# Performance work log

Hardware: AMD Instinct MI355X
Metric: run time of the kernel (lower is better)

Reference implementation:

```python
import jax, jax.numpy as jnp
import numpy as np
import math

B, S, DIM = 32, 1, 4096
NH, NKV, HD = 32, 8, 128
MAXLEN = 4096
START_POS = 4095


def _rope(t, freqs):
    # t: (b, s, h, hd); freqs: (s, hd//2, 2) = (cos/real, sin/imag)
    b, s, h, hd = t.shape
    tr = t.astype(jnp.float32).reshape(b, s, h, hd // 2, 2)
    c = freqs[None, :, None, :, 0]
    sn = freqs[None, :, None, :, 1]
    x0, x1 = tr[..., 0], tr[..., 1]
    out = jnp.stack([x0 * c - x1 * sn, x0 * sn + x1 * c], axis=-1)
    return out.reshape(b, s, h, hd).astype(t.dtype)


def setup_inputs() -> dict:
    key = jax.random.key(0)
    ks = jax.random.split(key, 8)
    sd = 1.0 / math.sqrt(DIM)
    x = jax.random.normal(ks[0], (B, S, DIM), dtype=jnp.float32)
    freqs = jax.random.normal(ks[1], (S, HD // 2, 2), dtype=jnp.float32)
    cache_k = jax.random.normal(ks[2], (B, MAXLEN, NKV, HD), dtype=jnp.float32)
    cache_v = jax.random.normal(ks[3], (B, MAXLEN, NKV, HD), dtype=jnp.float32)
    wq = jax.random.normal(ks[4], (NH * HD, DIM), dtype=jnp.float32) * sd
    wk = jax.random.normal(ks[5], (NKV * HD, DIM), dtype=jnp.float32) * sd
    wv = jax.random.normal(ks[6], (NKV * HD, DIM), dtype=jnp.float32) * sd
    wo = jax.random.normal(ks[7], (DIM, NH * HD), dtype=jnp.float32) * sd
    return {"x": x, "freqs": freqs, "cache_k": cache_k, "cache_v": cache_v,
            "wq": wq, "wk": wk, "wv": wv, "wo": wo, "start_pos": START_POS}


def reference(x, freqs, cache_k, cache_v, wq, wk, wv, wo, start_pos):
    b, s, _ = x.shape
    n_rep = NH // NKV
    xq = (x @ wq.T).reshape(b, s, NH, HD)
    xk = (x @ wk.T).reshape(b, s, NKV, HD)
    xv = (x @ wv.T).reshape(b, s, NKV, HD)
    xq = _rope(xq, freqs)
    xk = _rope(xk, freqs)
    # KV-cache write then read of prefix (static start_pos)
    keys = cache_k.at[:, start_pos:start_pos + s].set(xk)[:, :start_pos + s]
    values = cache_v.at[:, start_pos:start_pos + s].set(xv)[:, :start_pos + s]
    # GQA: group q heads (g=NKV kv groups, r=n_rep) without materializing repeat
    q = xq.reshape(b, s, NKV, n_rep, HD)
    scores = jnp.einsum('bsgrd,blgd->bgrsl', q, keys) / math.sqrt(HD)
    probs = jax.nn.softmax(scores.astype(jnp.float32), axis=-1).astype(xq.dtype)
    out = jnp.einsum('bgrsl,blgd->bsgrd', probs, values).reshape(b, s, NH * HD)
    return out @ wo.T
```

## Files before the change

### kernel.cpp

```cpp
#include <hip/hip_runtime.h>

#define QSCALE 0.08838834764831845f


typedef float f32x4 __attribute__((ext_vector_type(4)));

__device__ __forceinline__ float4 ntload4(const float* p) {
    const f32x4 v = __builtin_nontemporal_load((const f32x4*)p);
    return make_float4(v.x, v.y, v.z, v.w);
}

#define GEMM_FMA(r, wf) \
    acc[r][0] = fmaf(wf.x, x0.x, acc[r][0]); acc[r][0] = fmaf(wf.y, x0.y, acc[r][0]); \
    acc[r][0] = fmaf(wf.z, x0.z, acc[r][0]); acc[r][0] = fmaf(wf.w, x0.w, acc[r][0]); \
    acc[r][1] = fmaf(wf.x, x1.x, acc[r][1]); acc[r][1] = fmaf(wf.y, x1.y, acc[r][1]); \
    acc[r][1] = fmaf(wf.z, x1.z, acc[r][1]); acc[r][1] = fmaf(wf.w, x1.w, acc[r][1]); \
    acc[r][2] = fmaf(wf.x, x2.x, acc[r][2]); acc[r][2] = fmaf(wf.y, x2.y, acc[r][2]); \
    acc[r][2] = fmaf(wf.z, x2.z, acc[r][2]); acc[r][2] = fmaf(wf.w, x2.w, acc[r][2]); \
    acc[r][3] = fmaf(wf.x, x3.x, acc[r][3]); acc[r][3] = fmaf(wf.y, x3.y, acc[r][3]); \
    acc[r][3] = fmaf(wf.z, x3.z, acc[r][3]); acc[r][3] = fmaf(wf.w, x3.w, acc[r][3]);

__device__ __forceinline__ void gemv3(
    const float* __restrict__ W,
    const float* __restrict__ X,
    float* __restrict__ part, const int M, const int m0, const int ks)
{
    const int t = threadIdx.x;
    const int ksub = t & 3;
    const int ngrp = (t >> 2) & 7;
    const int mgrp = t >> 5;

    const int kbase = ks * 256 + ksub * 4;
    const float* wr0 = W + (size_t)(mgrp * 8 + 0) * 4096 + kbase;
    const float* wr1 = W + (size_t)(mgrp * 8 + 1) * 4096 + kbase;
    const float* wr2 = W + (size_t)(mgrp * 8 + 2) * 4096 + kbase;
    const float* wr3 = W + (size_t)(mgrp * 8 + 3) * 4096 + kbase;
    const float* wr4 = W + (size_t)(mgrp * 8 + 4) * 4096 + kbase;
    const float* wr5 = W + (size_t)(mgrp * 8 + 5) * 4096 + kbase;
    const float* wr6 = W + (size_t)(mgrp * 8 + 6) * 4096 + kbase;
    const float* wr7 = W + (size_t)(mgrp * 8 + 7) * 4096 + kbase;
    const float* xr0 = X + (size_t)(ngrp * 4 + 0) * 4096 + kbase;
    const float* xr1 = X + (size_t)(ngrp * 4 + 1) * 4096 + kbase;
    const float* xr2 = X + (size_t)(ngrp * 4 + 2) * 4096 + kbase;
    const float* xr3 = X + (size_t)(ngrp * 4 + 3) * 4096 + kbase;

    float acc[8][4];
#pragma unroll
    for (int r = 0; r < 8; ++r)
#pragma unroll
        for (int n = 0; n < 4; ++n) acc[r][n] = 0.f;

#pragma unroll 2
    for (int c = 0; c < 16; ++c) {
        const int off = c * 16;
        const float4 w0 = *(const float4*)(wr0 + off);
        const float4 w1 = *(const float4*)(wr1 + off);
        const float4 w2 = *(const float4*)(wr2 + off);
        const float4 w3 = *(const float4*)(wr3 + off);
        const float4 w4 = *(const float4*)(wr4 + off);
        const float4 w5 = *(const float4*)(wr5 + off);
        const float4 w6 = *(const float4*)(wr6 + off);
        const float4 w7 = *(const float4*)(wr7 + off);
        const float4 x0 = *(const float4*)(xr0 + off);
        const float4 x1 = *(const float4*)(xr1 + off);
        const float4 x2 = *(const float4*)(xr2 + off);
        const float4 x3 = *(const float4*)(xr3 + off);
        GEMM_FMA(0, w0) GEMM_FMA(1, w1) GEMM_FMA(2, w2) GEMM_FMA(3, w3)
        GEMM_FMA(4, w4) GEMM_FMA(5, w5) GEMM_FMA(6, w6) GEMM_FMA(7, w7)
    }

#pragma unroll
    for (int r = 0; r < 8; ++r)
#pragma unroll
        for (int n = 0; n < 4; ++n) {
            acc[r][n] += __shfl_xor(acc[r][n], 1);
            acc[r][n] += __shfl_xor(acc[r][n], 2);
        }

    if (ksub == 0) {
        float* base = part + (size_t)ks * 32 * M + m0 + mgrp * 8;
#pragma unroll
        for (int n = 0; n < 4; ++n) {
            float* dst = base + (size_t)(ngrp * 4 + n) * M;
            *(float4*)(dst)     = make_float4(acc[0][n], acc[1][n], acc[2][n], acc[3][n]);
            *(float4*)(dst + 4) = make_float4(acc[4][n], acc[5][n], acc[6][n], acc[7][n]);
        }
    }
}

__global__ __launch_bounds__(256, 4) void gemv_qkv_kernel(
    const float* __restrict__ wq, const float* __restrict__ wk,
    const float* __restrict__ wv, const float* __restrict__ x,
    float* __restrict__ part)
{
    const int mb = blockIdx.x >> 4, ks = blockIdx.x & 15;
    const int m0 = mb * 64;
    const float* W;
    if (m0 < 4096)      W = wq + (size_t)m0 * 4096;
    else if (m0 < 5120) W = wk + (size_t)(m0 - 4096) * 4096;
    else                W = wv + (size_t)(m0 - 5120) * 4096;
    gemv3(W, x, part, 6144, m0, ks);
}

__global__ __launch_bounds__(256, 4) void gemv_out_kernel(
    const float* __restrict__ wo, const float* __restrict__ a_ws,
    float* __restrict__ part)
{
    const int mb = blockIdx.x >> 4, ks = blockIdx.x & 15;
    gemv3(wo + (size_t)(mb * 64) * 4096, a_ws, part, 4096, mb * 64, ks);
}

__global__ __launch_bounds__(256) void qkv_combine_kernel(
    const float* __restrict__ part,
    const float* __restrict__ freqs,
    float* __restrict__ qc_g, float* __restrict__ kn_g, float* __restrict__ vn_g)
{
    const int idx = blockIdx.x * 256 + threadIdx.x;
    const int b = idx / 1536;
    const int cm = (idx - b * 1536) * 4;
    const float* p = part + (size_t)b * 6144 + cm;
    float4 v = make_float4(0.f, 0.f, 0.f, 0.f);
#pragma unroll
    for (int s = 0; s < 16; ++s) {
        const float4 a = *(const float4*)(p + (size_t)s * (32 * 6144));
        v.x += a.x; v.y += a.y; v.z += a.z; v.w += a.w;
    }
    if (cm < 4096) {
        const int d = cm & 127;
        const float4 f = *(const float4*)(freqs + d);
        float4 o;
        o.x = (v.x * f.x - v.y * f.y) * QSCALE;
        o.y = (v.x * f.y + v.y * f.x) * QSCALE;
        o.z = (v.z * f.z - v.w * f.w) * QSCALE;
        o.w = (v.z * f.w + v.w * f.z) * QSCALE;
        *(float4*)(qc_g + (size_t)b * 4096 + cm) = o;
    } else if (cm < 5120) {
        const int d = (cm - 4096) & 127;
        const float4 f = *(const float4*)(freqs + d);
        float4 o;
        o.x = v.x * f.x - v.y * f.y;
        o.y = v.x * f.y + v.y * f.x;
        o.z = v.z * f.z - v.w * f.w;
        o.w = v.z * f.w + v.w * f.z;
        *(float4*)(kn_g + (size_t)b * 1024 + (cm - 4096)) = o;
    } else {
        *(float4*)(vn_g + (size_t)b * 1024 + (cm - 5120)) = v;
    }
}

__global__ __launch_bounds__(256, 4) void attn7_kernel(
    const float* __restrict__ qc_g, const float* __restrict__ kn_g,
    const float* __restrict__ vn_g,
    const float* __restrict__ cache_k, const float* __restrict__ cache_v,
    float* __restrict__ pmss, float* __restrict__ pacc)
{
    const int t = threadIdx.x;
    const int w = t >> 6, lane = t & 63;
    const int g2 = lane >> 5, j = lane & 31;
    const int o3 = j & 3;
    const int bid = blockIdx.x;
    const int q2 = bid & 1, split = (bid >> 1) & 15, b = bid >> 5;
    const int gsub = w >> 1, rsub = w & 1;
    const int g = q2 * 4 + gsub * 2 + g2;
    const int row0 = split * 256 + rsub * 128;

    float4 q[4];
    const float* qb = qc_g + (size_t)b * 4096 + (size_t)g * 512 + j * 4;
#pragma unroll
    for (int h = 0; h < 4; ++h) q[h] = *(const float4*)(qb + h * 128);

    float m_s = -1e30f, ss_s = 0.f;
    float4 acc[4];
#pragma unroll
    for (int s = 0; s < 4; ++s) acc[s] = make_float4(0.f, 0.f, 0.f, 0.f);

    auto process = [&](const float4 kf, const float4 vf) {
        float d[4];
#pragma unroll
        for (int h = 0; h < 4; ++h)
            d[h] = fmaf(q[h].x, kf.x, fmaf(q[h].y, kf.y,
                   fmaf(q[h].z, kf.z, q[h].w * kf.w)));
        d[0] += __shfl_xor(d[0], 1); d[1] += __shfl_xor(d[1], 1);
        d[2] += __shfl_xor(d[2], 1); d[3] += __shfl_xor(d[3], 1);
        d[0] += __shfl_xor(d[0], 2); d[1] += __shfl_xor(d[1], 2);
        d[2] += __shfl_xor(d[2], 2); d[3] += __shfl_xor(d[3], 2);
        const float t0 = (o3 & 1) ? d[1] : d[0];
        const float t1 = (o3 & 1) ? d[3] : d[2];
        float dsc = (o3 & 2) ? t1 : t0;
        dsc += __shfl_xor(dsc, 4);
        dsc += __shfl_xor(dsc, 8);
        dsc += __shfl_xor(dsc, 16);
        if (__any(dsc - m_s > 8.0f)) {
            const float nm = fmaxf(m_s, dsc);
            const float c  = __expf(m_s - nm);
            m_s = nm; ss_s *= c;
            const float c1 = __shfl_xor(c, 1);
            const float c2 = __shfl_xor(c, 2);
            const float c3 = __shfl_xor(c1, 2);
            acc[0].x *= c;  acc[0].y *= c;  acc[0].z *= c;  acc[0].w *= c;
            acc[1].x *= c1; acc[1].y *= c1; acc[1].z *= c1; acc[1].w *= c1;
            acc[2].x *= c2; acc[2].y *= c2; acc[2].z *= c2; acc[2].w *= c2;
            acc[3].x *= c3; acc[3].y *= c3; acc[3].z *= c3; acc[3].w *= c3;
        }
        const float pe = __expf(dsc - m_s);
        ss_s += pe;
        const float p1 = __shfl_xor(pe, 1);
        const float p2 = __shfl_xor(pe, 2);
        const float p3 = __shfl_xor(p1, 2);
        acc[0].x = fmaf(pe, vf.x, acc[0].x); acc[0].y = fmaf(pe, vf.y, acc[0].y);
        acc[0].z = fmaf(pe, vf.z, acc[0].z); acc[0].w = fmaf(pe, vf.w, acc[0].w);
        acc[1].x = fmaf(p1, vf.x, acc[1].x); acc[1].y = fmaf(p1, vf.y, acc[1].y);
        acc[1].z = fmaf(p1, vf.z, acc[1].z); acc[1].w = fmaf(p1, vf.w, acc[1].w);
        acc[2].x = fmaf(p2, vf.x, acc[2].x); acc[2].y = fmaf(p2, vf.y, acc[2].y);
        acc[2].z = fmaf(p2, vf.z, acc[2].z); acc[2].w = fmaf(p2, vf.w, acc[2].w);
        acc[3].x = fmaf(p3, vf.x, acc[3].x); acc[3].y = fmaf(p3, vf.y, acc[3].y);
        acc[3].z = fmaf(p3, vf.z, acc[3].z); acc[3].w = fmaf(p3, vf.w, acc[3].w);
    };

    const size_t cbase = ((size_t)b * 4096 + row0) * 1024 + (size_t)g * 128 + j * 4;
    const float* kp = cache_k + cbase;
    const float* vp = cache_v + cbase;

    const bool lastw = (split == 15) && (rsub == 1);
    const int n = lastw ? 127 : 128;

    float4 kA, vA, kB, vB, kC, vC, kD, vD;
    kA = ntload4(kp);        vA = ntload4(vp);
    kB = ntload4(kp + 1024); vB = ntload4(vp + 1024);
    int i = 0;
    for (; i + 4 <= n; i += 4) {
        const float* k2 = kp + (size_t)(i + 2) * 1024;
        const float* v2 = vp + (size_t)(i + 2) * 1024;
        kC = ntload4(k2);        vC = ntload4(v2);
        kD = ntload4(k2 + 1024); vD = ntload4(v2 + 1024);
        process(kA, vA);
        process(kB, vB);
        if (i + 6 <= n) {
            const float* k4 = kp + (size_t)(i + 4) * 1024;
            const float* v4 = vp + (size_t)(i + 4) * 1024;
            kA = ntload4(k4);        vA = ntload4(v4);
            kB = ntload4(k4 + 1024); vB = ntload4(v4 + 1024);
        } else if (i + 5 <= n) {
            const float* k4 = kp + (size_t)(i + 4) * 1024;
            const float* v4 = vp + (size_t)(i + 4) * 1024;
            kA = ntload4(k4); vA = ntload4(v4);
        }
        process(kC, vC);
        process(kD, vD);
    }
    if (i < n)     process(kA, vA);
    if (i + 1 < n) process(kB, vB);
    if (i + 2 < n) {
        const float4 kf = ntload4(kp + (size_t)(i + 2) * 1024);
        const float4 vf = ntload4(vp + (size_t)(i + 2) * 1024);
        process(kf, vf);
    }
    if (lastw) {
        const float4 kf = *(const float4*)(kn_g + (size_t)b * 1024 + (size_t)g * 128 + j * 4);
        const float4 vf = *(const float4*)(vn_g + (size_t)b * 1024 + (size_t)g * 128 + j * 4);
        process(kf, vf);
    }

    const int pidx = (((b * 16 + split) * 2 + rsub) * 8 + g) * 4;
#pragma unroll
    for (int s = 0; s < 4; ++s) {
        const int head = o3 ^ s;
        *(float4*)(pacc + (size_t)(pidx + head) * 128 + j * 4) = acc[s];
    }
    if (j < 4) {
        pmss[(size_t)(pidx + j) * 2]     = m_s;
        pmss[(size_t)(pidx + j) * 2 + 1] = ss_s;
    }
}

__global__ __launch_bounds__(128) void attn_combine_kernel(
    const float* __restrict__ pmss, const float* __restrict__ pacc,
    float* __restrict__ a_ws)
{
    const int bg = blockIdx.x, t = threadIdx.x;
    const int h = t >> 5, jj = t & 31;
    const int b = bg >> 3, g = bg & 7;

    float M = -1e30f;
#pragma unroll
    for (int s = 0; s < 16; ++s)
#pragma unroll
        for (int r = 0; r < 2; ++r) {
            const int idx = (((b * 16 + s) * 2 + r) * 8 + g) * 4 + h;
            M = fmaxf(M, pmss[(size_t)idx * 2]);
        }
    float SS = 0.f;
    float4 o = make_float4(0.f, 0.f, 0.f, 0.f);
#pragma unroll
    for (int s = 0; s < 16; ++s)
#pragma unroll
        for (int r = 0; r < 2; ++r) {
            const int idx = (((b * 16 + s) * 2 + r) * 8 + g) * 4 + h;
            const float wgt = __expf(pmss[(size_t)idx * 2] - M);
            SS = fmaf(pmss[(size_t)idx * 2 + 1], wgt, SS);
            const float4 a = *(const float4*)(pacc + (size_t)idx * 128 + jj * 4);
            o.x = fmaf(a.x, wgt, o.x);
            o.y = fmaf(a.y, wgt, o.y);
            o.z = fmaf(a.z, wgt, o.z);
            o.w = fmaf(a.w, wgt, o.w);
        }
    const float inv = 1.f / SS;
    o.x *= inv; o.y *= inv; o.z *= inv; o.w *= inv;
    *(float4*)&a_ws[(size_t)b * 4096 + (size_t)(g * 4 + h) * 128 + jj * 4] = o;
}

__global__ __launch_bounds__(256) void out_combine_kernel(
    const float* __restrict__ part, float* __restrict__ out)
{
    const int i4 = (blockIdx.x * 256 + threadIdx.x) * 4;
    float4 v = make_float4(0.f, 0.f, 0.f, 0.f);
#pragma unroll
    for (int s = 0; s < 16; ++s) {
        const float4 a = *(const float4*)(part + (size_t)s * 131072 + i4);
        v.x += a.x; v.y += a.y; v.z += a.z; v.w += a.w;
    }
    *(float4*)(out + i4) = v;
}

extern "C" void kernel_launch(void* const* d_in, const int* in_sizes, int n_in,
                              void* d_out, int out_size, void* d_ws, size_t ws_size,
                              hipStream_t stream)
{
    const float* x       = (const float*)d_in[0];
    const float* freqs   = (const float*)d_in[1];
    const float* cache_k = (const float*)d_in[2];
    const float* cache_v = (const float*)d_in[3];
    const float* wq      = (const float*)d_in[4];
    const float* wk      = (const float*)d_in[5];
    const float* wv      = (const float*)d_in[6];
    const float* wo      = (const float*)d_in[7];

    float* out = (float*)d_out;
    float* ws  = (float*)d_ws;
    float* part_qkv = ws;
    float* qc_g     = ws + 3145728;
    float* kn_g     = ws + 3276800;
    float* vn_g     = ws + 3309568;
    float* pmss     = ws + 3342336;
    float* pacc     = ws + 3407872;
    float* a_ws     = ws + 7602176;
    float* part_out = ws + 7733248;

    gemv_qkv_kernel<<<1536, 256, 0, stream>>>(wq, wk, wv, x, part_qkv);
    qkv_combine_kernel<<<192, 256, 0, stream>>>(part_qkv, freqs, qc_g, kn_g, vn_g);
    attn7_kernel<<<1024, 256, 0, stream>>>(qc_g, kn_g, vn_g, cache_k, cache_v, pmss, pacc);
    attn_combine_kernel<<<256, 128, 0, stream>>>(pmss, pacc, a_ws);
    gemv_out_kernel<<<1024, 256, 0, stream>>>(wo, a_ws, part_out);
    out_combine_kernel<<<128, 256, 0, stream>>>(part_out, out);
}
```

Baseline: 280.5 us.

## Double attention split count and shrink prefetch depth in decode attention

Splits the KV sequence into 32 chunks per batch instead of 16, launching twice as many attention blocks with 64 rows per wave, and raises the launch-bounds occupancy hint from 4 to 5. The load pipeline drops from four rows in flight to two, which lowers register pressure so more waves can be resident to hide memory latency. The combine kernel and workspace offsets are resized to handle twice as many partial results, adding extra partial-sum traffic and combine work in exchange.

```diff
diff --git a/kernel.cpp b/kernel.cpp
--- a/kernel.cpp
+++ b/kernel.cpp
@@ -148,7 +148,7 @@
     }
 }
 
-__global__ __launch_bounds__(256, 4) void attn7_kernel(
+__global__ __launch_bounds__(256, 5) void attn9_kernel(
     const float* __restrict__ qc_g, const float* __restrict__ kn_g,
     const float* __restrict__ vn_g,
     const float* __restrict__ cache_k, const float* __restrict__ cache_v,
@@ -159,10 +159,10 @@
     const int g2 = lane >> 5, j = lane & 31;
     const int o3 = j & 3;
     const int bid = blockIdx.x;
-    const int q2 = bid & 1, split = (bid >> 1) & 15, b = bid >> 5;
+    const int q2 = bid & 1, split = (bid >> 1) & 31, b = bid >> 6;
     const int gsub = w >> 1, rsub = w & 1;
     const int g = q2 * 4 + gsub * 2 + g2;
-    const int row0 = split * 256 + rsub * 128;
+    const int row0 = split * 128 + rsub * 64;
 
     float4 q[4];
     const float* qb = qc_g + (size_t)b * 4096 + (size_t)g * 512 + j * 4;
@@ -221,47 +221,30 @@
     const float* kp = cache_k + cbase;
     const float* vp = cache_v + cbase;
 
-    const bool lastw = (split == 15) && (rsub == 1);
-    const int n = lastw ? 127 : 128;
-
-    float4 kA, vA, kB, vB, kC, vC, kD, vD;
-    kA = ntload4(kp);        vA = ntload4(vp);
-    kB = ntload4(kp + 1024); vB = ntload4(vp + 1024);
+    const bool lastw = (split == 31) && (rsub == 1);
+    const int n = lastw ? 63 : 64;
+
+    float4 kA, vA, kB, vB;
+    kA = ntload4(kp); vA = ntload4(vp);
     int i = 0;
-    for (; i + 4 <= n; i += 4) {
-        const float* k2 = kp + (size_t)(i + 2) * 1024;
-        const float* v2 = vp + (size_t)(i + 2) * 1024;
-        kC = ntload4(k2);        vC = ntload4(v2);
-        kD = ntload4(k2 + 1024); vD = ntload4(v2 + 1024);
+    for (; i + 2 <= n; i += 2) {
+        kB = ntload4(kp + (size_t)(i + 1) * 1024);
+        vB = ntload4(vp + (size_t)(i + 1) * 1024);
         process(kA, vA);
+        if (i + 2 < n) {
+            kA = ntload4(kp + (size_t)(i + 2) * 1024);
+            vA = ntload4(vp + (size_t)(i + 2) * 1024);
+        }
         process(kB, vB);
-        if (i + 6 <= n) {
-            const float* k4 = kp + (size_t)(i + 4) * 1024;
-            const float* v4 = vp + (size_t)(i + 4) * 1024;
-            kA = ntload4(k4);        vA = ntload4(v4);
-            kB = ntload4(k4 + 1024); vB = ntload4(v4 + 1024);
-        } else if (i + 5 <= n) {
-            const float* k4 = kp + (size_t)(i + 4) * 1024;
-            const float* v4 = vp + (size_t)(i + 4) * 1024;
-            kA = ntload4(k4); vA = ntload4(v4);
-        }
-        process(kC, vC);
-        process(kD, vD);
-    }
-    if (i < n)     process(kA, vA);
-    if (i + 1 < n) process(kB, vB);
-    if (i + 2 < n) {
-        const float4 kf = ntload4(kp + (size_t)(i + 2) * 1024);
-        const float4 vf = ntload4(vp + (size_t)(i + 2) * 1024);
-        process(kf, vf);
-    }
+    }
+    if (i < n) process(kA, vA);
     if (lastw) {
         const float4 kf = *(const float4*)(kn_g + (size_t)b * 1024 + (size_t)g * 128 + j * 4);
         const float4 vf = *(const float4*)(vn_g + (size_t)b * 1024 + (size_t)g * 128 + j * 4);
         process(kf, vf);
     }
 
-    const int pidx = (((b * 16 + split) * 2 + rsub) * 8 + g) * 4;
+    const int pidx = (((b * 32 + split) * 2 + rsub) * 8 + g) * 4;
 #pragma unroll
     for (int s = 0; s < 4; ++s) {
         const int head = o3 ^ s;
@@ -283,19 +266,19 @@
 
     float M = -1e30f;
 #pragma unroll
-    for (int s = 0; s < 16; ++s)
+    for (int s = 0; s < 32; ++s)
 #pragma unroll
         for (int r = 0; r < 2; ++r) {
-            const int idx = (((b * 16 + s) * 2 + r) * 8 + g) * 4 + h;
+            const int idx = (((b * 32 + s) * 2 + r) * 8 + g) * 4 + h;
             M = fmaxf(M, pmss[(size_t)idx * 2]);
         }
     float SS = 0.f;
     float4 o = make_float4(0.f, 0.f, 0.f, 0.f);
 #pragma unroll
-    for (int s = 0; s < 16; ++s)
+    for (int s = 0; s < 32; ++s)
 #pragma unroll
         for (int r = 0; r < 2; ++r) {
-            const int idx = (((b * 16 + s) * 2 + r) * 8 + g) * 4 + h;
+            const int idx = (((b * 32 + s) * 2 + r) * 8 + g) * 4 + h;
             const float wgt = __expf(pmss[(size_t)idx * 2] - M);
             SS = fmaf(pmss[(size_t)idx * 2 + 1], wgt, SS);
             const float4 a = *(const float4*)(pacc + (size_t)idx * 128 + jj * 4);
@@ -342,13 +325,13 @@
     float* kn_g     = ws + 3276800;
     float* vn_g     = ws + 3309568;
     float* pmss     = ws + 3342336;
-    float* pacc     = ws + 3407872;
-    float* a_ws     = ws + 7602176;
-    float* part_out = ws + 7733248;
+    float* pacc     = ws + 3473408;
+    float* a_ws     = ws + 11862016;
+    float* part_out = ws + 11993088;
 
     gemv_qkv_kernel<<<1536, 256, 0, stream>>>(wq, wk, wv, x, part_qkv);
     qkv_combine_kernel<<<192, 256, 0, stream>>>(part_qkv, freqs, qc_g, kn_g, vn_g);
-    attn7_kernel<<<1024, 256, 0, stream>>>(qc_g, kn_g, vn_g, cache_k, cache_v, pmss, pacc);
+    attn9_kernel<<<2048, 256, 0, stream>>>(qc_g, kn_g, vn_g, cache_k, cache_v, pmss, pacc);
     attn_combine_kernel<<<256, 128, 0, stream>>>(pmss, pacc, a_ws);
     gemv_out_kernel<<<1024, 256, 0, stream>>>(wo, a_ws, part_out);
     out_combine_kernel<<<128, 256, 0, stream>>>(part_out, out);
```

Result: slower. 298.7 us (+6.5%).
